# Optimization experiments

Measured on AMD Instinct MI355X. Metric: run time of the kernel, lower is better.

## Reference

```python
import jax, jax.numpy as jnp
import numpy as np

N = 50000          # nodes
E_RAND = 800000    # random edges (plus N self-loops)
IN, HID, OUT = 128, 32, 32
HEADS = (4, 4, 6)
NEG_SLOPE = 0.2    # DGL GATConv default leaky_relu slope


def setup_inputs() -> dict:
    key = jax.random.key(0)
    ks = jax.random.split(key, 16)
    s = 0.05
    x = jax.random.normal(ks[0], (N, IN), jnp.float32)
    # random graph + self loops (SELF_LOOP=True in the source)
    src = jnp.concatenate([jax.random.randint(ks[1], (E_RAND,), 0, N),
                           jnp.arange(N)]).astype(jnp.int32)
    dst = jnp.concatenate([jax.random.randint(ks[2], (E_RAND,), 0, N),
                           jnp.arange(N)]).astype(jnp.int32)
    H0, H1, H2 = HEADS
    return dict(
        x=x, src=src, dst=dst,
        W1=jax.random.normal(ks[3], (IN, H0 * HID), jnp.float32) * s,
        al1=jax.random.normal(ks[4], (H0, HID), jnp.float32) * s,
        ar1=jax.random.normal(ks[5], (H0, HID), jnp.float32) * s,
        b1=jnp.zeros((H0 * HID,), jnp.float32),
        W2=jax.random.normal(ks[6], (H0 * HID, H1 * HID), jnp.float32) * s,
        al2=jax.random.normal(ks[7], (H1, HID), jnp.float32) * s,
        ar2=jax.random.normal(ks[8], (H1, HID), jnp.float32) * s,
        b2=jnp.zeros((H1 * HID,), jnp.float32),
        W3=jax.random.normal(ks[9], (H1 * HID, H2 * OUT), jnp.float32) * s,
        al3=jax.random.normal(ks[10], (H2, OUT), jnp.float32) * s,
        ar3=jax.random.normal(ks[11], (H2, OUT), jnp.float32) * s,
        b3=jnp.zeros((H2 * OUT,), jnp.float32),
        resW3=jax.random.normal(ks[12], (H1 * HID, H2 * OUT), jnp.float32) * s,
    )


def gat_layer(h, src, dst, W, al, ar, b, residual=None, act_relu=True):
    """One DGL-style GATConv: fc -> per-edge leaky_relu attention -> edge
    softmax over incoming edges -> weighted scatter-sum -> (+res) + bias -> act."""
    n = h.shape[0]
    H, out = al.shape
    feat = (h @ W).reshape(n, H, out)                 # [N,H,out]
    el = jnp.sum(feat * al, axis=-1)                  # [N,H]
    er = jnp.sum(feat * ar, axis=-1)                  # [N,H]
    e = jax.nn.leaky_relu(el[src] + er[dst], NEG_SLOPE)  # [E,H]
    emax = jax.ops.segment_max(e, dst, num_segments=n)   # [N,H]
    ex = jnp.exp(e - emax[dst])                       # [E,H]
    denom = jax.ops.segment_sum(ex, dst, num_segments=n) # [N,H]
    alpha = ex / jnp.maximum(denom[dst], 1e-9)        # [E,H]
    msg = feat[src] * alpha[..., None]                # [E,H,out]
    rst = jax.ops.segment_sum(msg, dst, num_segments=n)  # [N,H,out]
    if residual is not None:
        rst = rst + residual
    rst = rst + b.reshape(1, H, out)
    return jax.nn.relu(rst) if act_relu else rst


def reference(x, src, dst, W1, al1, ar1, b1, W2, al2, ar2, b2,
              W3, al3, ar3, b3, resW3):
    n = x.shape[0]
    # layer 1: no residual, relu, flatten heads
    h1 = gat_layer(x, src, dst, W1, al1, ar1, b1).reshape(n, -1)
    # layer 2: residual is Identity (in_dim == heads*hid), relu, flatten
    res2 = h1.reshape(n, HEADS[1], HID)
    h2 = gat_layer(h1, src, dst, W2, al2, ar2, b2, residual=res2).reshape(n, -1)
    # layer 3: residual via linear projection (dims differ), no activation, mean heads
    res3 = (h2 @ resW3).reshape(n, HEADS[2], OUT)
    h3 = gat_layer(h2, src, dst, W3, al3, ar3, b3, residual=res3, act_relu=False)
    return h3.mean(axis=1)
```

## Files before the change

### kernel.cpp

```cpp
#include <hip/hip_runtime.h>
#include <math.h>


typedef _Float16 v8h __attribute__((ext_vector_type(8)));
typedef float f32x4 __attribute__((ext_vector_type(4)));

__device__ __host__ inline int pack_off(int n, int k) {
    return ((n >> 4) << 11) | ((k >> 5) << 9) | (((k >> 3) & 3) << 7) | ((n & 15) << 3) | (k & 7);
}


__global__ void hist_kernel(const int* __restrict__ dst, int E, int* __restrict__ deg) {
    int i = blockIdx.x * blockDim.x + threadIdx.x;
    if (i < E) atomicAdd(&deg[dst[i]], 1);
}

__global__ void scan_phaseA(const int* __restrict__ deg, int n, int* __restrict__ bsum) {
    __shared__ int red[4];
    int t = threadIdx.x;
    int base = blockIdx.x * 2048 + t * 8;
    int s = 0;
    #pragma unroll
    for (int q = 0; q < 8; q++) { int i = base + q; if (i < n) s += deg[i]; }
    #pragma unroll
    for (int off = 1; off < 64; off <<= 1) s += __shfl_xor(s, off);
    if ((t & 63) == 0) red[t >> 6] = s;
    __syncthreads();
    if (t == 0) bsum[blockIdx.x] = red[0] + red[1] + red[2] + red[3];
}

__global__ void scan_phaseB(int* __restrict__ bsum, int nb) {
    int lane = threadIdx.x & 63;
    int v = (lane < nb) ? bsum[lane] : 0;
    int inc = v;
    #pragma unroll
    for (int off = 1; off < 64; off <<= 1) {
        int u = __shfl_up(inc, off);
        if (lane >= off) inc += u;
    }
    int ex = inc - v;
    if (lane < nb) bsum[lane] = ex;
}

__global__ void scan_phaseC(const int* __restrict__ deg, int n, const int* __restrict__ bsum,
                            int* __restrict__ row_start, int E) {
    __shared__ int wsum[4];
    int t = threadIdx.x;
    int lane = t & 63, wv = t >> 6;
    int base = blockIdx.x * 2048 + t * 8;
    int v[8]; int s = 0;
    #pragma unroll
    for (int q = 0; q < 8; q++) { int i = base + q; v[q] = (i < n) ? deg[i] : 0; s += v[q]; }
    int inc = s;
    #pragma unroll
    for (int off = 1; off < 64; off <<= 1) {
        int u = __shfl_up(inc, off);
        if (lane >= off) inc += u;
    }
    if (lane == 63) wsum[wv] = inc;
    __syncthreads();
    int woff = 0;
    for (int w = 0; w < wv; w++) woff += wsum[w];
    int run = inc - s + woff + bsum[blockIdx.x];
    #pragma unroll
    for (int q = 0; q < 8; q++) {
        int i = base + q;
        if (i < n) row_start[i] = run;
        run += v[q];
    }
    if (blockIdx.x == 0 && t == 0) row_start[n] = E;
}

__global__ void fill_kernel(const int* __restrict__ src, const int* __restrict__ dst, int E,
                            const int* __restrict__ row_start, int* __restrict__ cursor,
                            int* __restrict__ csr_src) {
    int i = blockIdx.x * blockDim.x + threadIdx.x;
    if (i < E) {
        int d = dst[i];
        int pos = atomicAdd(&cursor[d], 1);
        csr_src[row_start[d] + pos] = src[i];
    }
}


__global__ void wsplit_all(const float* __restrict__ W1, const float* __restrict__ W2,
                           const float* __restrict__ W3, const float* __restrict__ Wr,
                           _Float16* __restrict__ o) {
    int i = blockIdx.x * blockDim.x + threadIdx.x;
    if (i >= 61440) return;
    float v; int ohi, stride, po;
    if (i < 16384) {
        int e = i, c = e >> 7, k = e & 127;
        v = W1[(size_t)k * 128 + c]; ohi = 0; stride = 16384; po = pack_off(c, k);
    } else if (i < 32768) {
        int e = i - 16384, c = e >> 7, k = e & 127;
        v = W2[(size_t)k * 128 + c]; ohi = 32768; stride = 16384; po = pack_off(c, k);
    } else if (i < 57344) {
        int e = i - 32768, c = e >> 7, k = e & 127;
        v = W3[(size_t)k * 192 + c]; ohi = 65536; stride = 28672; po = pack_off(c, k);
    } else {
        int e = i - 57344, c = e >> 7, k = e & 127;
        float s = 0.f;
        #pragma unroll
        for (int h = 0; h < 6; h++) s += Wr[(size_t)k * 192 + h * 32 + c];
        v = s * (1.0f / 6.0f);
        ohi = 65536; stride = 28672; po = 24576 + pack_off(c, k);
    }
    _Float16 hv = (_Float16)v;
    o[ohi + po] = hv;
    o[ohi + stride + po] = (_Float16)(v - (float)hv);
}


__global__ void splitx_kernel(const float* __restrict__ x, _Float16* __restrict__ hi,
                              _Float16* __restrict__ lo, int N, int PT) {
    int i = blockIdx.x * blockDim.x + threadIdx.x;
    if (i >= PT * 2048) return;
    int mt = i >> 11, r = i & 2047;
    int q4 = r >> 9, quad = (r >> 7) & 3, ln = (r >> 3) & 15, j = r & 7;
    int n = mt * 16 + ln, k = q4 * 32 + quad * 8 + j;
    float v = (n < N) ? x[(size_t)n * 128 + k] : 0.f;
    _Float16 h = (_Float16)v;
    hi[i] = h;
    lo[i] = (_Float16)(v - (float)h);
}


template <int CC, int H>
__global__ __launch_bounds__(256, 4) void mfma_fc(
    const _Float16* __restrict__ Ahi, const _Float16* __restrict__ Alo,
    const _Float16* __restrict__ Bhi, const _Float16* __restrict__ Blo,
    const float* __restrict__ al, const float* __restrict__ ar,
    _Float16* __restrict__ feat_out,
    float* __restrict__ el, float* __restrict__ er, int N) {
    constexpr int TILES = CC / 16;
    int t = threadIdx.x;
    int wave = t >> 6, lane = t & 63;
    int ln = lane & 15, quad = lane >> 4;
    int mt = blockIdx.x * 4 + wave;

    f32x4 acc[TILES];
    #pragma unroll
    for (int i = 0; i < TILES; i++) acc[i] = (f32x4){0.f, 0.f, 0.f, 0.f};

    const _Float16* pa_h = Ahi + (size_t)mt * 2048 + lane * 8;
    const _Float16* pa_l = Alo + (size_t)mt * 2048 + lane * 8;

    #pragma unroll
    for (int q4 = 0; q4 < 4; q4++) {
        v8h ah = *(const v8h*)(pa_h + q4 * 512);
        v8h av = *(const v8h*)(pa_l + q4 * 512);
        #pragma unroll
        for (int tt = 0; tt < TILES; tt++) {
            size_t boff = (size_t)tt * 2048 + q4 * 512 + lane * 8;
            v8h bh = *(const v8h*)(Bhi + boff);
            v8h bl = *(const v8h*)(Blo + boff);
            acc[tt] = __builtin_amdgcn_mfma_f32_16x16x32_f16(av, bh, acc[tt], 0, 0, 0);
            acc[tt] = __builtin_amdgcn_mfma_f32_16x16x32_f16(ah, bl, acc[tt], 0, 0, 0);
            acc[tt] = __builtin_amdgcn_mfma_f32_16x16x32_f16(ah, bh, acc[tt], 0, 0, 0);
        }
    }

    #pragma unroll
    for (int tt = 0; tt < TILES; tt++) {
        int n = tt * 16 + ln;
        int head = n >> 5, wi = n & 31;
        _Float16* fo = feat_out + (size_t)head * N * 32;
        #pragma unroll
        for (int r = 0; r < 4; r++) {
            int m = mt * 16 + quad * 4 + r;
            if (m < N) fo[(size_t)m * 32 + wi] = (_Float16)acc[tt][r];
        }
    }
    #pragma unroll
    for (int hg = 0; hg < H; hg++) {
        float a0 = al[hg * 32 + ln], a1 = al[hg * 32 + 16 + ln];
        float r0 = ar[hg * 32 + ln], r1 = ar[hg * 32 + 16 + ln];
        #pragma unroll
        for (int r = 0; r < 4; r++) {
            float pl = acc[2 * hg][r] * a0 + acc[2 * hg + 1][r] * a1;
            float pr = acc[2 * hg][r] * r0 + acc[2 * hg + 1][r] * r1;
            #pragma unroll
            for (int off = 1; off < 16; off <<= 1) {
                pl += __shfl_xor(pl, off);
                pr += __shfl_xor(pr, off);
            }
            int m = mt * 16 + quad * 4 + r;
            if (ln == 0 && m < N) {
                el[(size_t)hg * N + m] = pl;
                er[(size_t)hg * N + m] = pr;
            }
        }
    }
}


__global__ __launch_bounds__(256, 3) void mfma_fc3(
    const _Float16* __restrict__ Ahi, const _Float16* __restrict__ Alo,
    const _Float16* __restrict__ Bhi, const _Float16* __restrict__ Blo,
    const float* __restrict__ al, const float* __restrict__ ar,
    _Float16* __restrict__ feat_out, float* __restrict__ res_m,
    float* __restrict__ el, float* __restrict__ er, int N) {
    constexpr int CC = 192, H = 6, TILES = 14;
    int t = threadIdx.x;
    int wave = t >> 6, lane = t & 63;
    int ln = lane & 15, quad = lane >> 4;
    int mt = blockIdx.x * 4 + wave;

    f32x4 acc[TILES];
    #pragma unroll
    for (int i = 0; i < TILES; i++) acc[i] = (f32x4){0.f, 0.f, 0.f, 0.f};

    const _Float16* pa_h = Ahi + (size_t)mt * 2048 + lane * 8;
    const _Float16* pa_l = Alo + (size_t)mt * 2048 + lane * 8;

    #pragma unroll
    for (int q4 = 0; q4 < 4; q4++) {
        v8h ah = *(const v8h*)(pa_h + q4 * 512);
        v8h av = *(const v8h*)(pa_l + q4 * 512);
        #pragma unroll
        for (int tt = 0; tt < TILES; tt++) {
            size_t boff = (size_t)tt * 2048 + q4 * 512 + lane * 8;
            v8h bh = *(const v8h*)(Bhi + boff);
            v8h bl = *(const v8h*)(Blo + boff);
            acc[tt] = __builtin_amdgcn_mfma_f32_16x16x32_f16(av, bh, acc[tt], 0, 0, 0);
            acc[tt] = __builtin_amdgcn_mfma_f32_16x16x32_f16(ah, bl, acc[tt], 0, 0, 0);
            acc[tt] = __builtin_amdgcn_mfma_f32_16x16x32_f16(ah, bh, acc[tt], 0, 0, 0);
        }
    }

    #pragma unroll
    for (int tt = 0; tt < 12; tt++) {
        int n = tt * 16 + ln;
        #pragma unroll
        for (int r = 0; r < 4; r++) {
            int m = mt * 16 + quad * 4 + r;
            if (m < N) feat_out[(size_t)m * CC + n] = (_Float16)acc[tt][r];
        }
    }
    #pragma unroll
    for (int tt = 12; tt < 14; tt++) {
        int n32 = (tt - 12) * 16 + ln;
        #pragma unroll
        for (int r = 0; r < 4; r++) {
            int m = mt * 16 + quad * 4 + r;
            if (m < N) res_m[(size_t)m * 32 + n32] = acc[tt][r];
        }
    }
    #pragma unroll
    for (int hg = 0; hg < H; hg++) {
        float a0 = al[hg * 32 + ln], a1 = al[hg * 32 + 16 + ln];
        float r0 = ar[hg * 32 + ln], r1 = ar[hg * 32 + 16 + ln];
        #pragma unroll
        for (int r = 0; r < 4; r++) {
            float pl = acc[2 * hg][r] * a0 + acc[2 * hg + 1][r] * a1;
            float pr = acc[2 * hg][r] * r0 + acc[2 * hg + 1][r] * r1;
            #pragma unroll
            for (int off = 1; off < 16; off <<= 1) {
                pl += __shfl_xor(pl, off);
                pr += __shfl_xor(pr, off);
            }
            int m = mt * 16 + quad * 4 + r;
            if (ln == 0 && m < N) {
                el[(size_t)hg * N + m] = pl;
                er[(size_t)hg * N + m] = pr;
            }
        }
    }
}


template <int RES>
__global__ __launch_bounds__(256) void gat_agg_q(
        const _Float16* __restrict__ feat_planes, const float* __restrict__ el,
        const float* __restrict__ er, const int* __restrict__ row_start,
        const int* __restrict__ csr_src, const float* __restrict__ bias,
        const _Float16* __restrict__ res_hi, const _Float16* __restrict__ res_lo,
        _Float16* __restrict__ out_hi, _Float16* __restrict__ out_lo,
        int N, int NB16) {
    constexpr int H = 4;
    unsigned b = blockIdx.x;
    unsigned C = (unsigned)(NB16 * H) >> 3;
    unsigned t = (b & 7u) * C + (b >> 3);
    int h  = (int)(t / (unsigned)NB16);
    int ng = (int)(t - (unsigned)h * (unsigned)NB16);
    int wv = threadIdx.x >> 6, lane = threadIdx.x & 63;
    int slice = lane >> 4, sl = lane & 15;
    int q = sl & 3;
    int g = sl >> 2;
    int n = ng * 16 + wv * 4 + slice;
    bool valid = (n < N);
    int nc = valid ? n : (N - 1);

    int start = row_start[nc];
    int end   = valid ? row_start[nc + 1] : start;
    float er_h = er[(size_t)h * N + nc];
    const float* el_h = el + (size_t)h * N;
    const _Float16* fbase = feat_planes + (size_t)h * N * 32 + q * 8;

    float acc[8];
    #pragma unroll
    for (int i = 0; i < 8; i++) acc[i] = 0.f;
    float wsum = 0.f;

    int j = start + g;
    for (; j + 4 < end; j += 8) {
        int s0 = csr_src[j];
        int s1 = csr_src[j + 4];
        float e0 = el_h[s0] + er_h;
        float e1 = el_h[s1] + er_h;
        e0 = (e0 >= 0.f) ? e0 : 0.2f * e0;
        e1 = (e1 >= 0.f) ? e1 : 0.2f * e1;
        float w0 = __expf(e0);
        float w1 = __expf(e1);
        v8h v0 = *(const v8h*)(fbase + (size_t)s0 * 32);
        v8h v1 = *(const v8h*)(fbase + (size_t)s1 * 32);
        wsum += w0 + w1;
        #pragma unroll
        for (int i = 0; i < 8; i++) acc[i] += w0 * (float)v0[i] + w1 * (float)v1[i];
    }
    if (j < end) {
        int s0 = csr_src[j];
        float e0 = el_h[s0] + er_h;
        e0 = (e0 >= 0.f) ? e0 : 0.2f * e0;
        float w0 = __expf(e0);
        v8h v0 = *(const v8h*)(fbase + (size_t)s0 * 32);
        wsum += w0;
        #pragma unroll
        for (int i = 0; i < 8; i++) acc[i] += w0 * (float)v0[i];
    }

    #pragma unroll
    for (int off = 4; off < 16; off <<= 1) {
        #pragma unroll
        for (int i = 0; i < 8; i++) acc[i] += __shfl_xor(acc[i], off);
        wsum += __shfl_xor(wsum, off);
    }

    float inv = 1.0f / fmaxf(wsum, 1e-9f);
    float4 bv0 = *(const float4*)(bias + h * 32 + q * 8);
    float4 bv1 = *(const float4*)(bias + h * 32 + q * 8 + 4);
    float r[8];
    r[0] = acc[0] * inv + bv0.x; r[1] = acc[1] * inv + bv0.y;
    r[2] = acc[2] * inv + bv0.z; r[3] = acc[3] * inv + bv0.w;
    r[4] = acc[4] * inv + bv1.x; r[5] = acc[5] * inv + bv1.y;
    r[6] = acc[6] * inv + bv1.z; r[7] = acc[7] * inv + bv1.w;

    if constexpr (RES == 1) {
        int off = pack_off(nc, h * 32 + q * 8);
        v8h rh = *(const v8h*)(res_hi + off);
        v8h rl = *(const v8h*)(res_lo + off);
        #pragma unroll
        for (int i = 0; i < 8; i++) r[i] += (float)rh[i] + (float)rl[i];
    }
    #pragma unroll
    for (int i = 0; i < 8; i++) r[i] = fmaxf(r[i], 0.f);

    if (g == 0 && valid) {
        int po = pack_off(n, h * 32 + q * 8);
        v8h hh, ll;
        #pragma unroll
        for (int i = 0; i < 8; i++) {
            hh[i] = (_Float16)r[i];
            ll[i] = (_Float16)(r[i] - (float)hh[i]);
        }
        *(v8h*)(out_hi + po) = hh;
        *(v8h*)(out_lo + po) = ll;
    }
}


__global__ __launch_bounds__(256) void gat_agg_mean6(
        const _Float16* __restrict__ feat, const float* __restrict__ el,
        const float* __restrict__ er, const int* __restrict__ row_start,
        const int* __restrict__ csr_src, const float* __restrict__ bias,
        const float* __restrict__ res_m, float* __restrict__ out, int N) {
    constexpr int H = 6, ROW = 192, LPG = 24, G = 2;
    int wv = threadIdx.x >> 6, lane = threadIdx.x & 63;
    int n = blockIdx.x * 4 + wv;
    if (n >= N) return;

    int d8 = lane % LPG;
    int g  = lane / LPG;
    int hd = d8 >> 2;

    int start = row_start[n], end = row_start[n + 1];
    float er_hd = er[(size_t)hd * N + n];
    const float* el_h = el + (size_t)hd * N;
    const _Float16* fbase = feat + 8 * d8;

    float acc[8];
    #pragma unroll
    for (int q = 0; q < 8; q++) acc[q] = 0.f;
    float wsum = 0.f;

    int j = (g < G) ? (start + g) : end;
    for (; j + G < end; j += 2 * G) {
        int s0 = csr_src[j];
        int s1 = csr_src[j + G];
        float e0 = el_h[s0] + er_hd;
        float e1 = el_h[s1] + er_hd;
        e0 = (e0 >= 0.f) ? e0 : 0.2f * e0;
        e1 = (e1 >= 0.f) ? e1 : 0.2f * e1;
        float w0 = __expf(e0);
        float w1 = __expf(e1);
        v8h v0 = *(const v8h*)(fbase + (size_t)s0 * ROW);
        v8h v1 = *(const v8h*)(fbase + (size_t)s1 * ROW);
        wsum += w0 + w1;
        #pragma unroll
        for (int q = 0; q < 8; q++) acc[q] += w0 * (float)v0[q] + w1 * (float)v1[q];
    }
    if (j < end) {
        int s0 = csr_src[j];
        float e0 = el_h[s0] + er_hd;
        e0 = (e0 >= 0.f) ? e0 : 0.2f * e0;
        float w0 = __expf(e0);
        v8h v0 = *(const v8h*)(fbase + (size_t)s0 * ROW);
        wsum += w0;
        #pragma unroll
        for (int q = 0; q < 8; q++) acc[q] += w0 * (float)v0[q];
    }

    #pragma unroll
    for (int q = 0; q < 8; q++) acc[q] += __shfl(acc[q], lane + 24);
    wsum += __shfl(wsum, lane + 24);

    float inv = 1.0f / fmaxf(wsum, 1e-9f);
    float4 bv0 = *(const float4*)(bias + 8 * d8);
    float4 bv1 = *(const float4*)(bias + 8 * d8 + 4);
    float r[8];
    r[0] = acc[0] * inv + bv0.x; r[1] = acc[1] * inv + bv0.y;
    r[2] = acc[2] * inv + bv0.z; r[3] = acc[3] * inv + bv0.w;
    r[4] = acc[4] * inv + bv1.x; r[5] = acc[5] * inv + bv1.y;
    r[6] = acc[6] * inv + bv1.z; r[7] = acc[7] * inv + bv1.w;

    int qb = d8 & 3;
    float s[8];
    #pragma unroll
    for (int q = 0; q < 8; q++) {
        s[q] = r[q];
        #pragma unroll
        for (int hh2 = 1; hh2 < H; hh2++) s[q] += __shfl(r[q], qb + 4 * hh2);
    }
    if (lane < 4) {
        const float sc = 1.0f / 6.0f;
        float4 rm0 = *(const float4*)(res_m + (size_t)n * 32 + 8 * lane);
        float4 rm1 = *(const float4*)(res_m + (size_t)n * 32 + 8 * lane + 4);
        *(float4*)(out + (size_t)n * 32 + 8 * lane) =
            make_float4(s[0] * sc + rm0.x, s[1] * sc + rm0.y,
                        s[2] * sc + rm0.z, s[3] * sc + rm0.w);
        *(float4*)(out + (size_t)n * 32 + 8 * lane + 4) =
            make_float4(s[4] * sc + rm1.x, s[5] * sc + rm1.y,
                        s[6] * sc + rm1.z, s[7] * sc + rm1.w);
    }
}


extern "C" void kernel_launch(void* const* d_in, const int* in_sizes, int n_in,
                              void* d_out, int out_size, void* d_ws, size_t ws_size,
                              hipStream_t stream) {
    const float* x    = (const float*)d_in[0];
    const int*   src  = (const int*)d_in[1];
    const int*   dst  = (const int*)d_in[2];
    const float* W1   = (const float*)d_in[3];
    const float* al1  = (const float*)d_in[4];
    const float* ar1  = (const float*)d_in[5];
    const float* b1   = (const float*)d_in[6];
    const float* W2   = (const float*)d_in[7];
    const float* al2  = (const float*)d_in[8];
    const float* ar2  = (const float*)d_in[9];
    const float* b2   = (const float*)d_in[10];
    const float* W3   = (const float*)d_in[11];
    const float* al3  = (const float*)d_in[12];
    const float* ar3  = (const float*)d_in[13];
    const float* b3   = (const float*)d_in[14];
    const float* resW3= (const float*)d_in[15];
    float* out = (float*)d_out;

    const int N = in_sizes[0] / 128;
    const int E = in_sizes[1];
    const int TILES16 = (N + 15) / 16;
    const int PT = (TILES16 + 3) & ~3;
    const int NB = PT / 4;
    const int NSB = (N + 2047) / 2048;
    const int NB16 = (((N + 15) / 16) + 1) & ~1;

    float* fws  = (float*)d_ws;
    float* res_m = fws;
    float* elb  = res_m + (size_t)N * 32;
    float* erb  = elb + (size_t)N * 6;
    _Float16* feat_h = (_Float16*)(erb + (size_t)N * 6);
    _Float16* xh_hi  = feat_h + (size_t)N * 192;
    _Float16* xh_lo  = xh_hi + (size_t)PT * 2048;
    _Float16* h1_hi  = xh_lo + (size_t)PT * 2048;
    _Float16* h1_lo  = h1_hi + (size_t)PT * 2048;
    _Float16* wts    = h1_lo + (size_t)PT * 2048;
    int* deg       = (int*)(wts + 122880);
    int* row_start = deg + N;
    int* bsum      = row_start + (N + 1);
    int* csr_src   = bsum + 64;

    const _Float16* W1h = wts;
    const _Float16* W1l = wts + 16384;
    const _Float16* W2h = wts + 32768;
    const _Float16* W2l = wts + 49152;
    const _Float16* B3h = wts + 65536;
    const _Float16* B3l = wts + 94208;

    hipMemsetAsync(deg, 0, (size_t)N * sizeof(int), stream);
    hist_kernel<<<dim3((E + 255) / 256), dim3(256), 0, stream>>>(dst, E, deg);
    scan_phaseA<<<dim3(NSB), dim3(256), 0, stream>>>(deg, N, bsum);
    scan_phaseB<<<dim3(1), dim3(64), 0, stream>>>(bsum, NSB);
    scan_phaseC<<<dim3(NSB), dim3(256), 0, stream>>>(deg, N, bsum, row_start, E);
    hipMemsetAsync(deg, 0, (size_t)N * sizeof(int), stream);
    fill_kernel<<<dim3((E + 255) / 256), dim3(256), 0, stream>>>(src, dst, E, row_start, deg, csr_src);
    wsplit_all<<<dim3(240), dim3(256), 0, stream>>>(W1, W2, W3, resW3, wts);
    splitx_kernel<<<dim3((PT * 2048 + 255) / 256), dim3(256), 0, stream>>>(x, xh_hi, xh_lo, N, PT);

    mfma_fc<128, 4><<<dim3(NB), dim3(256), 0, stream>>>(
        xh_hi, xh_lo, W1h, W1l, al1, ar1, feat_h, elb, erb, N);
    gat_agg_q<0><<<dim3(NB16 * 4), dim3(256), 0, stream>>>(
        feat_h, elb, erb, row_start, csr_src, b1,
        nullptr, nullptr, h1_hi, h1_lo, N, NB16);

    mfma_fc<128, 4><<<dim3(NB), dim3(256), 0, stream>>>(
        h1_hi, h1_lo, W2h, W2l, al2, ar2, feat_h, elb, erb, N);
    gat_agg_q<1><<<dim3(NB16 * 4), dim3(256), 0, stream>>>(
        feat_h, elb, erb, row_start, csr_src, b2,
        h1_hi, h1_lo, xh_hi, xh_lo, N, NB16);

    mfma_fc3<<<dim3(NB), dim3(256), 0, stream>>>(
        xh_hi, xh_lo, B3h, B3l, al3, ar3, feat_h, res_m, elb, erb, N);
    gat_agg_mean6<<<dim3((N + 3) / 4), dim3(256), 0, stream>>>(
        feat_h, elb, erb, row_start, csr_src, b3, res_m, out, N);
}
```

Measured before the change: 432.3 us.

## Reuse head-planar aggregation kernel for layer 3 with atomic mean into output

Layer 3 features are now stored per head as separate 32-wide planes, and the generic per-head aggregation kernel, templated on head count, replaces the dedicated six-head mean kernel. The fc3 kernel writes the residual projection plus the head-averaged bias straight into the output. The aggregation kernel then atomically adds each head's scaled contribution into that output. This drops the res_m buffer and its reread, and gives a more parallel, per-head-blocked gather, at the cost of float atomics contending on output rows and a non-deterministic summation order.

Result: slower. 630.5 us (+45.8%).

```diff
diff --git a/kernel.cpp b/kernel.cpp
--- a/kernel.cpp
+++ b/kernel.cpp
@@ -199,9 +199,10 @@
     const _Float16* __restrict__ Ahi, const _Float16* __restrict__ Alo,
     const _Float16* __restrict__ Bhi, const _Float16* __restrict__ Blo,
     const float* __restrict__ al, const float* __restrict__ ar,
-    _Float16* __restrict__ feat_out, float* __restrict__ res_m,
+    const float* __restrict__ b3,
+    _Float16* __restrict__ feat_out, float* __restrict__ out,
     float* __restrict__ el, float* __restrict__ er, int N) {
-    constexpr int CC = 192, H = 6, TILES = 14;
+    constexpr int H = 6, TILES = 14;
     int t = threadIdx.x;
     int wave = t >> 6, lane = t & 63;
     int ln = lane & 15, quad = lane >> 4;
@@ -232,19 +233,23 @@
     #pragma unroll
     for (int tt = 0; tt < 12; tt++) {
         int n = tt * 16 + ln;
+        int head = n >> 5, wi = n & 31;
+        _Float16* fo = feat_out + (size_t)head * N * 32;
         #pragma unroll
         for (int r = 0; r < 4; r++) {
             int m = mt * 16 + quad * 4 + r;
-            if (m < N) feat_out[(size_t)m * CC + n] = (_Float16)acc[tt][r];
+            if (m < N) fo[(size_t)m * 32 + wi] = (_Float16)acc[tt][r];
         }
     }
     #pragma unroll
     for (int tt = 12; tt < 14; tt++) {
         int n32 = (tt - 12) * 16 + ln;
+        float bm = (b3[n32] + b3[32 + n32] + b3[64 + n32] + b3[96 + n32] +
+                    b3[128 + n32] + b3[160 + n32]) * (1.0f / 6.0f);
         #pragma unroll
         for (int r = 0; r < 4; r++) {
             int m = mt * 16 + quad * 4 + r;
-            if (m < N) res_m[(size_t)m * 32 + n32] = acc[tt][r];
+            if (m < N) out[(size_t)m * 32 + n32] = acc[tt][r] + bm;
         }
     }
     #pragma unroll
@@ -270,15 +275,15 @@
 }
 
 
-template <int RES>
+template <int H, int RES, int OUTMODE>
 __global__ __launch_bounds__(256) void gat_agg_q(
         const _Float16* __restrict__ feat_planes, const float* __restrict__ el,
         const float* __restrict__ er, const int* __restrict__ row_start,
         const int* __restrict__ csr_src, const float* __restrict__ bias,
         const _Float16* __restrict__ res_hi, const _Float16* __restrict__ res_lo,
         _Float16* __restrict__ out_hi, _Float16* __restrict__ out_lo,
+        float* __restrict__ out_f,
         int N, int NB16) {
-    constexpr int H = 4;
     unsigned b = blockIdx.x;
     unsigned C = (unsigned)(NB16 * H) >> 3;
     unsigned t = (b & 7u) * C + (b >> 3);
@@ -338,120 +343,44 @@
     }
 
     float inv = 1.0f / fmaxf(wsum, 1e-9f);
-    float4 bv0 = *(const float4*)(bias + h * 32 + q * 8);
-    float4 bv1 = *(const float4*)(bias + h * 32 + q * 8 + 4);
-    float r[8];
-    r[0] = acc[0] * inv + bv0.x; r[1] = acc[1] * inv + bv0.y;
-    r[2] = acc[2] * inv + bv0.z; r[3] = acc[3] * inv + bv0.w;
-    r[4] = acc[4] * inv + bv1.x; r[5] = acc[5] * inv + bv1.y;
-    r[6] = acc[6] * inv + bv1.z; r[7] = acc[7] * inv + bv1.w;
-
-    if constexpr (RES == 1) {
-        int off = pack_off(nc, h * 32 + q * 8);
-        v8h rh = *(const v8h*)(res_hi + off);
-        v8h rl = *(const v8h*)(res_lo + off);
-        #pragma unroll
-        for (int i = 0; i < 8; i++) r[i] += (float)rh[i] + (float)rl[i];
-    }
-    #pragma unroll
-    for (int i = 0; i < 8; i++) r[i] = fmaxf(r[i], 0.f);
-
-    if (g == 0 && valid) {
-        int po = pack_off(n, h * 32 + q * 8);
-        v8h hh, ll;
-        #pragma unroll
-        for (int i = 0; i < 8; i++) {
-            hh[i] = (_Float16)r[i];
-            ll[i] = (_Float16)(r[i] - (float)hh[i]);
-        }
-        *(v8h*)(out_hi + po) = hh;
-        *(v8h*)(out_lo + po) = ll;
-    }
-}
-
-
-__global__ __launch_bounds__(256) void gat_agg_mean6(
-        const _Float16* __restrict__ feat, const float* __restrict__ el,
-        const float* __restrict__ er, const int* __restrict__ row_start,
-        const int* __restrict__ csr_src, const float* __restrict__ bias,
-        const float* __restrict__ res_m, float* __restrict__ out, int N) {
-    constexpr int H = 6, ROW = 192, LPG = 24, G = 2;
-    int wv = threadIdx.x >> 6, lane = threadIdx.x & 63;
-    int n = blockIdx.x * 4 + wv;
-    if (n >= N) return;
-
-    int d8 = lane % LPG;
-    int g  = lane / LPG;
-    int hd = d8 >> 2;
-
-    int start = row_start[n], end = row_start[n + 1];
-    float er_hd = er[(size_t)hd * N + n];
-    const float* el_h = el + (size_t)hd * N;
-    const _Float16* fbase = feat + 8 * d8;
-
-    float acc[8];
-    #pragma unroll
-    for (int q = 0; q < 8; q++) acc[q] = 0.f;
-    float wsum = 0.f;
-
-    int j = (g < G) ? (start + g) : end;
-    for (; j + G < end; j += 2 * G) {
-        int s0 = csr_src[j];
-        int s1 = csr_src[j + G];
-        float e0 = el_h[s0] + er_hd;
-        float e1 = el_h[s1] + er_hd;
-        e0 = (e0 >= 0.f) ? e0 : 0.2f * e0;
-        e1 = (e1 >= 0.f) ? e1 : 0.2f * e1;
-        float w0 = __expf(e0);
-        float w1 = __expf(e1);
-        v8h v0 = *(const v8h*)(fbase + (size_t)s0 * ROW);
-        v8h v1 = *(const v8h*)(fbase + (size_t)s1 * ROW);
-        wsum += w0 + w1;
-        #pragma unroll
-        for (int q = 0; q < 8; q++) acc[q] += w0 * (float)v0[q] + w1 * (float)v1[q];
-    }
-    if (j < end) {
-        int s0 = csr_src[j];
-        float e0 = el_h[s0] + er_hd;
-        e0 = (e0 >= 0.f) ? e0 : 0.2f * e0;
-        float w0 = __expf(e0);
-        v8h v0 = *(const v8h*)(fbase + (size_t)s0 * ROW);
-        wsum += w0;
-        #pragma unroll
-        for (int q = 0; q < 8; q++) acc[q] += w0 * (float)v0[q];
-    }
-
-    #pragma unroll
-    for (int q = 0; q < 8; q++) acc[q] += __shfl(acc[q], lane + 24);
-    wsum += __shfl(wsum, lane + 24);
-
-    float inv = 1.0f / fmaxf(wsum, 1e-9f);
-    float4 bv0 = *(const float4*)(bias + 8 * d8);
-    float4 bv1 = *(const float4*)(bias + 8 * d8 + 4);
-    float r[8];
-    r[0] = acc[0] * inv + bv0.x; r[1] = acc[1] * inv + bv0.y;
-    r[2] = acc[2] * inv + bv0.z; r[3] = acc[3] * inv + bv0.w;
-    r[4] = acc[4] * inv + bv1.x; r[5] = acc[5] * inv + bv1.y;
-    r[6] = acc[6] * inv + bv1.z; r[7] = acc[7] * inv + bv1.w;
-
-    int qb = d8 & 3;
-    float s[8];
-    #pragma unroll
-    for (int q = 0; q < 8; q++) {
-        s[q] = r[q];
-        #pragma unroll
-        for (int hh2 = 1; hh2 < H; hh2++) s[q] += __shfl(r[q], qb + 4 * hh2);
-    }
-    if (lane < 4) {
-        const float sc = 1.0f / 6.0f;
-        float4 rm0 = *(const float4*)(res_m + (size_t)n * 32 + 8 * lane);
-        float4 rm1 = *(const float4*)(res_m + (size_t)n * 32 + 8 * lane + 4);
-        *(float4*)(out + (size_t)n * 32 + 8 * lane) =
-            make_float4(s[0] * sc + rm0.x, s[1] * sc + rm0.y,
-                        s[2] * sc + rm0.z, s[3] * sc + rm0.w);
-        *(float4*)(out + (size_t)n * 32 + 8 * lane + 4) =
-            make_float4(s[4] * sc + rm1.x, s[5] * sc + rm1.y,
-                        s[6] * sc + rm1.z, s[7] * sc + rm1.w);
+
+    if constexpr (OUTMODE == 1) {
+        float sc = inv * (1.0f / H);
+        if (g == 0 && valid) {
+            float* op = out_f + (size_t)n * 32 + q * 8;
+            #pragma unroll
+            for (int i = 0; i < 8; i++) atomicAdd(op + i, acc[i] * sc);
+        }
+    } else {
+        float4 bv0 = *(const float4*)(bias + h * 32 + q * 8);
+        float4 bv1 = *(const float4*)(bias + h * 32 + q * 8 + 4);
+        float r[8];
+        r[0] = acc[0] * inv + bv0.x; r[1] = acc[1] * inv + bv0.y;
+        r[2] = acc[2] * inv + bv0.z; r[3] = acc[3] * inv + bv0.w;
+        r[4] = acc[4] * inv + bv1.x; r[5] = acc[5] * inv + bv1.y;
+        r[6] = acc[6] * inv + bv1.z; r[7] = acc[7] * inv + bv1.w;
+
+        if constexpr (RES == 1) {
+            int off = pack_off(nc, h * 32 + q * 8);
+            v8h rh = *(const v8h*)(res_hi + off);
+            v8h rl = *(const v8h*)(res_lo + off);
+            #pragma unroll
+            for (int i = 0; i < 8; i++) r[i] += (float)rh[i] + (float)rl[i];
+        }
+        #pragma unroll
+        for (int i = 0; i < 8; i++) r[i] = fmaxf(r[i], 0.f);
+
+        if (g == 0 && valid) {
+            int po = pack_off(n, h * 32 + q * 8);
+            v8h hh, ll;
+            #pragma unroll
+            for (int i = 0; i < 8; i++) {
+                hh[i] = (_Float16)r[i];
+                ll[i] = (_Float16)(r[i] - (float)hh[i]);
+            }
+            *(v8h*)(out_hi + po) = hh;
+            *(v8h*)(out_lo + po) = ll;
+        }
     }
 }
 
@@ -483,11 +412,10 @@
     const int PT = (TILES16 + 3) & ~3;
     const int NB = PT / 4;
     const int NSB = (N + 2047) / 2048;
-    const int NB16 = (((N + 15) / 16) + 1) & ~1;
+    const int NB16 = (TILES16 + 3) & ~3;
 
     float* fws  = (float*)d_ws;
-    float* res_m = fws;
-    float* elb  = res_m + (size_t)N * 32;
+    float* elb  = fws;
     float* erb  = elb + (size_t)N * 6;
     _Float16* feat_h = (_Float16*)(erb + (size_t)N * 6);
     _Float16* xh_hi  = feat_h + (size_t)N * 192;
@@ -519,18 +447,19 @@
 
     mfma_fc<128, 4><<<dim3(NB), dim3(256), 0, stream>>>(
         xh_hi, xh_lo, W1h, W1l, al1, ar1, feat_h, elb, erb, N);
-    gat_agg_q<0><<<dim3(NB16 * 4), dim3(256), 0, stream>>>(
+    gat_agg_q<4, 0, 0><<<dim3(NB16 * 4), dim3(256), 0, stream>>>(
         feat_h, elb, erb, row_start, csr_src, b1,
-        nullptr, nullptr, h1_hi, h1_lo, N, NB16);
+        nullptr, nullptr, h1_hi, h1_lo, nullptr, N, NB16);
 
     mfma_fc<128, 4><<<dim3(NB), dim3(256), 0, stream>>>(
         h1_hi, h1_lo, W2h, W2l, al2, ar2, feat_h, elb, erb, N);
-    gat_agg_q<1><<<dim3(NB16 * 4), dim3(256), 0, stream>>>(
+    gat_agg_q<4, 1, 0><<<dim3(NB16 * 4), dim3(256), 0, stream>>>(
         feat_h, elb, erb, row_start, csr_src, b2,
-        h1_hi, h1_lo, xh_hi, xh_lo, N, NB16);
+        h1_hi, h1_lo, xh_hi, xh_lo, nullptr, N, NB16);
 
     mfma_fc3<<<dim3(NB), dim3(256), 0, stream>>>(
-        xh_hi, xh_lo, B3h, B3l, al3, ar3, feat_h, res_m, elb, erb, N);
-    gat_agg_mean6<<<dim3((N + 3) / 4), dim3(256), 0, stream>>>(
-        feat_h, elb, erb, row_start, csr_src, b3, res_m, out, N);
-}
+        xh_hi, xh_lo, B3h, B3l, al3, ar3, b3, feat_h, out, elb, erb, N);
+    gat_agg_q<6, 0, 1><<<dim3(NB16 * 6), dim3(256), 0, stream>>>(
+        feat_h, elb, erb, row_start, csr_src, nullptr,
+        nullptr, nullptr, nullptr, nullptr, out, N, NB16);
+}
```

## Store layer-3 features head-planar, fold bias into residual output, unroll aggregation

Applied to the files above, without the earlier changes.

Layer-3 FC now writes features as six per-head planes of 32 halves per node instead of 192-wide interleaved rows. It also writes residual plus mean bias directly into the output buffer, which removes the res_m workspace. The mean-6 aggregation gathers from the per-head planes, unrolls its edge loop four-deep for more loads in flight, and drops the per-lane bias loads. NB16 rounding also changes, which adds a few extra blocks to the agg_q grids.

After: 457.4 us. 1.06x slower.

```diff
diff --git a/kernel.cpp b/kernel.cpp
--- a/kernel.cpp
+++ b/kernel.cpp
@@ -199,9 +199,10 @@
     const _Float16* __restrict__ Ahi, const _Float16* __restrict__ Alo,
     const _Float16* __restrict__ Bhi, const _Float16* __restrict__ Blo,
     const float* __restrict__ al, const float* __restrict__ ar,
-    _Float16* __restrict__ feat_out, float* __restrict__ res_m,
+    const float* __restrict__ b3,
+    _Float16* __restrict__ feat_out, float* __restrict__ out,
     float* __restrict__ el, float* __restrict__ er, int N) {
-    constexpr int CC = 192, H = 6, TILES = 14;
+    constexpr int H = 6, TILES = 14;
     int t = threadIdx.x;
     int wave = t >> 6, lane = t & 63;
     int ln = lane & 15, quad = lane >> 4;
@@ -232,19 +233,23 @@
     #pragma unroll
     for (int tt = 0; tt < 12; tt++) {
         int n = tt * 16 + ln;
+        int head = n >> 5, wi = n & 31;
+        _Float16* fo = feat_out + (size_t)head * N * 32;
         #pragma unroll
         for (int r = 0; r < 4; r++) {
             int m = mt * 16 + quad * 4 + r;
-            if (m < N) feat_out[(size_t)m * CC + n] = (_Float16)acc[tt][r];
+            if (m < N) fo[(size_t)m * 32 + wi] = (_Float16)acc[tt][r];
         }
     }
     #pragma unroll
     for (int tt = 12; tt < 14; tt++) {
         int n32 = (tt - 12) * 16 + ln;
+        float bm = (b3[n32] + b3[32 + n32] + b3[64 + n32] + b3[96 + n32] +
+                    b3[128 + n32] + b3[160 + n32]) * (1.0f / 6.0f);
         #pragma unroll
         for (int r = 0; r < 4; r++) {
             int m = mt * 16 + quad * 4 + r;
-            if (m < N) res_m[(size_t)m * 32 + n32] = acc[tt][r];
+            if (m < N) out[(size_t)m * 32 + n32] = acc[tt][r] + bm;
         }
     }
     #pragma unroll
@@ -370,24 +375,23 @@
 }
 
 
-__global__ __launch_bounds__(256) void gat_agg_mean6(
-        const _Float16* __restrict__ feat, const float* __restrict__ el,
+__global__ __launch_bounds__(256) void gat_agg_mean6p(
+        const _Float16* __restrict__ feat_planes, const float* __restrict__ el,
         const float* __restrict__ er, const int* __restrict__ row_start,
-        const int* __restrict__ csr_src, const float* __restrict__ bias,
-        const float* __restrict__ res_m, float* __restrict__ out, int N) {
-    constexpr int H = 6, ROW = 192, LPG = 24, G = 2;
+        const int* __restrict__ csr_src, float* __restrict__ out, int N) {
+    constexpr int H = 6, LPG = 24, G = 2;
     int wv = threadIdx.x >> 6, lane = threadIdx.x & 63;
     int n = blockIdx.x * 4 + wv;
     if (n >= N) return;
 
     int d8 = lane % LPG;
     int g  = lane / LPG;
-    int hd = d8 >> 2;
+    int hd = d8 >> 2, qb = d8 & 3;
 
     int start = row_start[n], end = row_start[n + 1];
     float er_hd = er[(size_t)hd * N + n];
     const float* el_h = el + (size_t)hd * N;
-    const _Float16* fbase = feat + 8 * d8;
+    const _Float16* fbase = feat_planes + (size_t)hd * N * 32 + qb * 8;
 
     float acc[8];
     #pragma unroll
@@ -395,27 +399,39 @@
     float wsum = 0.f;
 
     int j = (g < G) ? (start + g) : end;
-    for (; j + G < end; j += 2 * G) {
+    for (; j + 3 * G < end; j += 4 * G) {
         int s0 = csr_src[j];
         int s1 = csr_src[j + G];
+        int s2 = csr_src[j + 2 * G];
+        int s3 = csr_src[j + 3 * G];
         float e0 = el_h[s0] + er_hd;
         float e1 = el_h[s1] + er_hd;
+        float e2 = el_h[s2] + er_hd;
+        float e3 = el_h[s3] + er_hd;
         e0 = (e0 >= 0.f) ? e0 : 0.2f * e0;
         e1 = (e1 >= 0.f) ? e1 : 0.2f * e1;
+        e2 = (e2 >= 0.f) ? e2 : 0.2f * e2;
+        e3 = (e3 >= 0.f) ? e3 : 0.2f * e3;
         float w0 = __expf(e0);
         float w1 = __expf(e1);
-        v8h v0 = *(const v8h*)(fbase + (size_t)s0 * ROW);
-        v8h v1 = *(const v8h*)(fbase + (size_t)s1 * ROW);
-        wsum += w0 + w1;
-        #pragma unroll
-        for (int q = 0; q < 8; q++) acc[q] += w0 * (float)v0[q] + w1 * (float)v1[q];
-    }
-    if (j < end) {
+        float w2 = __expf(e2);
+        float w3 = __expf(e3);
+        v8h v0 = *(const v8h*)(fbase + (size_t)s0 * 32);
+        v8h v1 = *(const v8h*)(fbase + (size_t)s1 * 32);
+        v8h v2 = *(const v8h*)(fbase + (size_t)s2 * 32);
+        v8h v3 = *(const v8h*)(fbase + (size_t)s3 * 32);
+        wsum += (w0 + w1) + (w2 + w3);
+        #pragma unroll
+        for (int q = 0; q < 8; q++)
+            acc[q] += (w0 * (float)v0[q] + w1 * (float)v1[q]) +
+                      (w2 * (float)v2[q] + w3 * (float)v3[q]);
+    }
+    for (; j < end; j += G) {
         int s0 = csr_src[j];
         float e0 = el_h[s0] + er_hd;
         e0 = (e0 >= 0.f) ? e0 : 0.2f * e0;
         float w0 = __expf(e0);
-        v8h v0 = *(const v8h*)(fbase + (size_t)s0 * ROW);
+        v8h v0 = *(const v8h*)(fbase + (size_t)s0 * 32);
         wsum += w0;
         #pragma unroll
         for (int q = 0; q < 8; q++) acc[q] += w0 * (float)v0[q];
@@ -426,15 +442,10 @@
     wsum += __shfl(wsum, lane + 24);
 
     float inv = 1.0f / fmaxf(wsum, 1e-9f);
-    float4 bv0 = *(const float4*)(bias + 8 * d8);
-    float4 bv1 = *(const float4*)(bias + 8 * d8 + 4);
     float r[8];
-    r[0] = acc[0] * inv + bv0.x; r[1] = acc[1] * inv + bv0.y;
-    r[2] = acc[2] * inv + bv0.z; r[3] = acc[3] * inv + bv0.w;
-    r[4] = acc[4] * inv + bv1.x; r[5] = acc[5] * inv + bv1.y;
-    r[6] = acc[6] * inv + bv1.z; r[7] = acc[7] * inv + bv1.w;
-
-    int qb = d8 & 3;
+    #pragma unroll
+    for (int q = 0; q < 8; q++) r[q] = acc[q] * inv;
+
     float s[8];
     #pragma unroll
     for (int q = 0; q < 8; q++) {
@@ -444,8 +455,8 @@
     }
     if (lane < 4) {
         const float sc = 1.0f / 6.0f;
-        float4 rm0 = *(const float4*)(res_m + (size_t)n * 32 + 8 * lane);
-        float4 rm1 = *(const float4*)(res_m + (size_t)n * 32 + 8 * lane + 4);
+        float4 rm0 = *(const float4*)(out + (size_t)n * 32 + 8 * lane);
+        float4 rm1 = *(const float4*)(out + (size_t)n * 32 + 8 * lane + 4);
         *(float4*)(out + (size_t)n * 32 + 8 * lane) =
             make_float4(s[0] * sc + rm0.x, s[1] * sc + rm0.y,
                         s[2] * sc + rm0.z, s[3] * sc + rm0.w);
@@ -483,11 +494,10 @@
     const int PT = (TILES16 + 3) & ~3;
     const int NB = PT / 4;
     const int NSB = (N + 2047) / 2048;
-    const int NB16 = (((N + 15) / 16) + 1) & ~1;
+    const int NB16 = (TILES16 + 3) & ~3;
 
     float* fws  = (float*)d_ws;
-    float* res_m = fws;
-    float* elb  = res_m + (size_t)N * 32;
+    float* elb  = fws;
     float* erb  = elb + (size_t)N * 6;
     _Float16* feat_h = (_Float16*)(erb + (size_t)N * 6);
     _Float16* xh_hi  = feat_h + (size_t)N * 192;
@@ -530,7 +540,7 @@
         h1_hi, h1_lo, xh_hi, xh_lo, N, NB16);
 
     mfma_fc3<<<dim3(NB), dim3(256), 0, stream>>>(
-        xh_hi, xh_lo, B3h, B3l, al3, ar3, feat_h, res_m, elb, erb, N);
-    gat_agg_mean6<<<dim3((N + 3) / 4), dim3(256), 0, stream>>>(
-        feat_h, elb, erb, row_start, csr_src, b3, res_m, out, N);
-}
+        xh_hi, xh_lo, B3h, B3l, al3, ar3, b3, feat_h, out, elb, erb, N);
+    gat_agg_mean6p<<<dim3((N + 3) / 4), dim3(256), 0, stream>>>(
+        feat_h, elb, erb, row_start, csr_src, out, N);
+}
```
